# Kernel tuning notes

Measured on AMD Instinct MI355X. Metric: run time of the kernel, lower is better.

## Reference

```python
import jax, jax.numpy as jnp
import numpy as np

B, N, F_IN, H, FO = 4, 2048, 256, 4, 64


def setup_inputs() -> dict:
    key = jax.random.key(0)
    k1, k2, k3, k4, k5 = jax.random.split(key, 5)
    x = jax.random.normal(k1, (B, N, F_IN), dtype=jnp.float32)
    # random 0/1 adjacency with self-loops so every row of softmax is finite
    adj = jax.random.randint(k2, (N, N), 0, 2).astype(jnp.float32)
    adj = jnp.maximum(adj, jnp.eye(N, dtype=jnp.float32))
    # parameters (xavier-uniform style)
    lim_w = float(np.sqrt(6.0 / (F_IN + H * FO)))
    W = jax.random.uniform(k3, (F_IN, H * FO), minval=-lim_w, maxval=lim_w, dtype=jnp.float32)
    lim_a = float(np.sqrt(6.0 / (H + FO)))
    a_src = jax.random.uniform(k4, (H, FO), minval=-lim_a, maxval=lim_a, dtype=jnp.float32)
    a_dst = jax.random.uniform(k5, (H, FO), minval=-lim_a, maxval=lim_a, dtype=jnp.float32)
    return {"x": x, "adj": adj, "W": W, "a_src": a_src, "a_dst": a_dst}


def reference(x, adj, W, a_src, a_dst):
    # h: (B, N, H, FO)
    h = (x @ W).reshape(B, N, H, FO)
    attn_src = jnp.einsum("bnhf,hf->bnh", h, a_src)  # (B,N,H)
    attn_dst = jnp.einsum("bnhf,hf->bnh", h, a_dst)  # (B,N,H)
    # scores[b,i,j,h] = src[b,i,h] + dst[b,j,h]
    scores = attn_src[:, :, None, :] + attn_dst[:, None, :, :]
    scores = jax.nn.leaky_relu(scores, negative_slope=0.2)
    mask = (adj == 0)[None, :, :, None]  # (1,N,N,1)
    scores = jnp.where(mask, -jnp.inf, scores)
    attn = jax.nn.softmax(scores, axis=2)  # softmax over neighbors j
    # dropout is identity in eval mode / p=0
    out = jnp.einsum("bijh,bjhf->bihf", attn, h)  # (B,N,H,FO)
    return out.reshape(B, N, H * FO)  # concat=True
```

## Files before the change

### kernel.cpp

```cpp
#include <hip/hip_runtime.h>
#include <hip/hip_bf16.h>
#include <math.h>

#define B 4
#define N 2048
#define FIN 256
#define H 4
#define FO 64
#define M (B*N)
#define HF (H*FO)

typedef __attribute__((ext_vector_type(8))) short short8;
typedef __attribute__((ext_vector_type(4))) float float4v;
typedef __attribute__((ext_vector_type(4))) int int4v;

#if __has_builtin(__builtin_amdgcn_exp2f)
#define EXP2(x) __builtin_amdgcn_exp2f(x)
#else
#define EXP2(x) exp2f(x)
#endif

static __device__ __forceinline__ unsigned int pk_rne(float a, float b) {
  unsigned int ua = __builtin_bit_cast(unsigned int, a);
  unsigned int ub = __builtin_bit_cast(unsigned int, b);
  ua += 0x7fffu + ((ua >> 16) & 1u);
  ub += 0x7fffu + ((ub >> 16) & 1u);
  return (ua >> 16) | (ub & 0xffff0000u);
}

static __device__ __forceinline__ unsigned int pk_trunc(float a, float b) {
#if __has_builtin(__builtin_amdgcn_perm)
  return __builtin_amdgcn_perm(__builtin_bit_cast(unsigned int, b),
                               __builtin_bit_cast(unsigned int, a), 0x07060302u);
#else
  return (__builtin_bit_cast(unsigned int, a) >> 16) |
         (__builtin_bit_cast(unsigned int, b) & 0xffff0000u);
#endif
}

static __device__ __forceinline__ void split_pair(float x0, float x1,
                                                  unsigned int& hi, unsigned int& lo) {
  unsigned int u0 = __builtin_bit_cast(unsigned int, x0);
  unsigned int u1 = __builtin_bit_cast(unsigned int, x1);
  hi = (u0 >> 16) | (u1 & 0xffff0000u);
  float h0 = __builtin_bit_cast(float, u0 & 0xffff0000u);
  float h1 = __builtin_bit_cast(float, u1 & 0xffff0000u);
  unsigned int l0 = __builtin_bit_cast(unsigned int, x0 - h0);
  unsigned int l1 = __builtin_bit_cast(unsigned int, x1 - h1);
  lo = (l0 >> 16) | (l1 & 0xffff0000u);
}

static __device__ __forceinline__ unsigned int fenc(float f) {
  unsigned int b = __builtin_bit_cast(unsigned int, f);
  return (b & 0x80000000u) ? ~b : (b | 0x80000000u);
}
static __device__ __forceinline__ float fdec(unsigned int e) {
  unsigned int b = (e & 0x80000000u) ? (e & 0x7fffffffu) : ~e;
  return __builtin_bit_cast(float, b);
}

__global__ __launch_bounds__(256) void prep_pack(const float* __restrict__ Wsrc,
                                                 const float* __restrict__ X,
                                                 const float* __restrict__ adj,
                                                 unsigned short* __restrict__ Wf_hi,
                                                 unsigned short* __restrict__ Wf_lo,
                                                 unsigned short* __restrict__ Xf_hi,
                                                 unsigned short* __restrict__ Xf_lo,
                                                 unsigned long long* __restrict__ packed,
                                                 unsigned int* __restrict__ DmaxEnc) {
  const int blk = blockIdx.x;
  const int t = threadIdx.x;
  if (blk >= 144) {
    const int row = blk - 144;
    const int w = t >> 6, l = t & 63;
    const float* ar = adj + (size_t)row * N;
    for (int c = w; c < N / 64; c += 4) {
      unsigned long long m = __ballot(ar[c * 64 + l] != 0.f);
      if (l == 0) packed[(size_t)row * (N / 64) + c] = m;
    }
    return;
  }
  __shared__ float lds[64][65];
  if (blk < 16) {
    if (blk == 0 && t < 16) DmaxEnc[t] = 0u;
    const int k0 = (blk >> 2) * 64;
    const int h  = blk & 3;
    const int n0 = h * 64;
    const int c4 = (t & 15) * 4;
    #pragma unroll
    for (int rep = 0; rep < 4; ++rep) {
      const int kl = (t >> 4) + 16 * rep;
      const float4 v = *(const float4*)(Wsrc + (size_t)(k0 + kl) * HF + n0 + c4);
      lds[kl][c4 + 0] = v.x; lds[kl][c4 + 1] = v.y;
      lds[kl][c4 + 2] = v.z; lds[kl][c4 + 3] = v.w;
    }
    __syncthreads();
    #pragma unroll
    for (int rep = 0; rep < 2; ++rep) {
      const int s   = t + rep * 256;
      const int kcl = s >> 8;
      const int tt  = (s >> 6) & 3;
      const int ln  = s & 63;
      const int fL  = tt * 16 + (ln & 15);
      const int kb  = kcl * 32 + (ln >> 4) * 8;
      unsigned int hv[4], lv[4];
      #pragma unroll
      for (int p = 0; p < 4; ++p)
        split_pair(lds[kb + 2 * p][fL], lds[kb + 2 * p + 1][fL], hv[p], lv[p]);
      const size_t off = ((((size_t)h * 8 + (k0 >> 5) + kcl) * 4 + tt) << 9) + ln * 8;
      *(uint4*)(Wf_hi + off) = make_uint4(hv[0], hv[1], hv[2], hv[3]);
      *(uint4*)(Wf_lo + off) = make_uint4(lv[0], lv[1], lv[2], lv[3]);
    }
    return;
  }
  const int xblk  = blk - 16;
  const int mrow0 = xblk * 64;
  for (int ktile = 0; ktile < 4; ++ktile) {
    if (ktile) __syncthreads();
    const int k0 = ktile * 64;
    const int c4 = (t & 15) * 4;
    #pragma unroll
    for (int rep = 0; rep < 4; ++rep) {
      const int rl = (t >> 4) + 16 * rep;
      const float4 v = *(const float4*)(X + (size_t)(mrow0 + rl) * FIN + k0 + c4);
      lds[rl][c4 + 0] = v.x; lds[rl][c4 + 1] = v.y;
      lds[rl][c4 + 2] = v.z; lds[rl][c4 + 3] = v.w;
    }
    __syncthreads();
    #pragma unroll
    for (int rep = 0; rep < 2; ++rep) {
      const int s   = t + rep * 256;
      const int mt  = s >> 7;
      const int kcl = (s >> 6) & 1;
      const int ln  = s & 63;
      const int mrl = mt * 16 + (ln & 15);
      const int kb  = kcl * 32 + (ln >> 4) * 8;
      unsigned int hv[4], lv[4];
      #pragma unroll
      for (int p = 0; p < 4; ++p)
        split_pair(lds[mrl][kb + 2 * p], lds[mrl][kb + 2 * p + 1], hv[p], lv[p]);
      const size_t off = (((size_t)(xblk * 4 + mt) * 8 + (ktile * 2 + kcl)) << 9) + ln * 8;
      *(uint4*)(Xf_hi + off) = make_uint4(hv[0], hv[1], hv[2], hv[3]);
      *(uint4*)(Xf_lo + off) = make_uint4(lv[0], lv[1], lv[2], lv[3]);
    }
  }
}

__global__ __launch_bounds__(256) void gemm_fused(const unsigned short* __restrict__ Xf_hi,
                                                  const unsigned short* __restrict__ Xf_lo,
                                                  const unsigned short* __restrict__ Wf_hi,
                                                  const unsigned short* __restrict__ Wf_lo,
                                                  const float* __restrict__ a_src,
                                                  const float* __restrict__ a_dst,
                                                  float* __restrict__ Srcv,
                                                  float2* __restrict__ Epair,
                                                  unsigned int* __restrict__ DmaxEnc,
                                                  unsigned short* __restrict__ Hf) {
  __shared__ unsigned short sh[64][72];
  __shared__ float smax[4];
  const int xcd  = blockIdx.x & 7;
  const int slot = blockIdx.x >> 3;
  const int mb = xcd * 16 + (slot >> 2);
  const int h  = slot & 3;
  const int w = threadIdx.x >> 6, lane = threadIdx.x & 63;
  const int fl = lane & 15, quad = lane >> 4;
  const float L2E = 1.4426950408889634f;

  const float4v zero = {0.f, 0.f, 0.f, 0.f};
  float4v acc[4] = {zero, zero, zero, zero};

  const size_t abase = (((size_t)(mb * 4 + w) * 8) << 9) + lane * 8;
  #pragma unroll
  for (int kc = 0; kc < 8; ++kc) {
    const short8 Ahi = *(const short8*)(Xf_hi + abase + ((size_t)kc << 9));
    const short8 Alo = *(const short8*)(Xf_lo + abase + ((size_t)kc << 9));
    #pragma unroll
    for (int t = 0; t < 4; ++t) {
      const size_t woff = ((((size_t)h * 8 + kc) * 4 + t) << 9) + lane * 8;
      const short8 Bhi = *(const short8*)(Wf_hi + woff);
      const short8 Blo = *(const short8*)(Wf_lo + woff);
      acc[t] = __builtin_amdgcn_mfma_f32_16x16x32_bf16(Ahi, Bhi, acc[t], 0, 0, 0);
      acc[t] = __builtin_amdgcn_mfma_f32_16x16x32_bf16(Alo, Bhi, acc[t], 0, 0, 0);
      acc[t] = __builtin_amdgcn_mfma_f32_16x16x32_bf16(Ahi, Blo, acc[t], 0, 0, 0);
    }
  }

  const int bb  = (mb * 64) >> 11;
  const int n0w = (mb * 64) & (N - 1);
  const int bh  = bb * H + h;
  float as[4], ad[4];
  #pragma unroll
  for (int t = 0; t < 4; ++t) {
    as[t] = a_src[h * FO + t * 16 + fl];
    ad[t] = a_dst[h * FO + t * 16 + fl];
  }
  float wmax = -INFINITY;
  #pragma unroll
  for (int reg = 0; reg < 4; ++reg) {
    float sv = 0.f, dv = 0.f;
    #pragma unroll
    for (int t = 0; t < 4; ++t) {
      sv = fmaf(acc[t][reg], as[t], sv);
      dv = fmaf(acc[t][reg], ad[t], dv);
    }
    #pragma unroll
    for (int off = 1; off <= 8; off <<= 1) {
      sv += __shfl_xor(sv, off, 64);
      dv += __shfl_xor(dv, off, 64);
    }
    wmax = fmaxf(wmax, dv);
    if (fl == 0) {
      const int node = n0w + w * 16 + quad * 4 + reg;
      Srcv[(bh << 11) + node] = sv;
      float2 e;
      e.x = EXP2(dv * L2E);
      e.y = EXP2(dv * (0.2f * L2E));
      Epair[(bh << 11) + node] = e;
    }
  }
  wmax = fmaxf(wmax, __shfl_xor(wmax, 16, 64));
  wmax = fmaxf(wmax, __shfl_xor(wmax, 32, 64));
  if (lane == 0) smax[w] = wmax;

  #pragma unroll
  for (int t = 0; t < 4; ++t) {
    const int nl = w * 16 + quad * 4;
    *(unsigned int*)&sh[t * 16 + fl][nl]     = pk_rne(acc[t][0], acc[t][1]);
    *(unsigned int*)&sh[t * 16 + fl][nl + 2] = pk_rne(acc[t][2], acc[t][3]);
  }
  __syncthreads();
  if (threadIdx.x == 0) {
    const float bmax = fmaxf(fmaxf(smax[0], smax[1]), fmaxf(smax[2], smax[3]));
    atomicMax(DmaxEnc + bh, fenc(bmax));
  }
  const int jc0 = n0w >> 5;
  #pragma unroll
  for (int rep = 0; rep < 2; ++rep) {
    const int s = (int)threadIdx.x + rep * 256;
    const int jcl = s >> 8;
    const int tt  = (s >> 6) & 3;
    const int ln  = s & 63;
    const int f    = tt * 16 + (ln & 15);
    const int node = jcl * 32 + (ln >> 4) * 8;
    unsigned short* dsth = Hf + (((size_t)bh * 64 + jc0 + jcl) * 4 + tt) * 512 + ln * 8;
    *(uint4*)dsth = *(const uint4*)&sh[f][node];
  }
}

__global__ __launch_bounds__(512) void gat_mfma(const unsigned char* __restrict__ pb,
                                                const float* __restrict__ Src,
                                                const float2* __restrict__ Epair,
                                                const unsigned int* __restrict__ DmaxEnc,
                                                const unsigned short* __restrict__ Hf,
                                                float* __restrict__ out) {
  const int xcd  = blockIdx.x & 7;
  const int slot = blockIdx.x >> 3;
  const int b    = xcd >> 1;
  const int i0   = ((xcd & 1) * 32 + slot) * 32;
  const int w    = threadIdx.x >> 6;
  const int lane = threadIdx.x & 63;
  const int h    = w & 3;
  const int jh   = w >> 2;
  const int bh   = b * H + h;
  const int fl   = lane & 15;
  const int kk   = (lane >> 4) * 8;
  const float L2E = 1.4426950408889634f;

  const int row0 = i0 + fl;
  const int row1 = i0 + 16 + fl;
  const float dmx = fdec(DmaxEnc[bh]);
  const float s0 = Src[(bh << 11) + row0];
  const float s1 = Src[(bh << 11) + row1];
  const float u0 = s0 + dmx, m0 = fmaxf(u0, 0.2f * u0);
  const float u1 = s1 + dmx, m1 = fmaxf(u1, 0.2f * u1);
  const float c1a = EXP2((s0 - m0) * L2E), c2a = EXP2((0.2f * s0 - m0) * L2E);
  const float c1b = EXP2((s1 - m1) * L2E), c2b = EXP2((0.2f * s1 - m1) * L2E);
  const float ta = EXP2(-s0 * L2E), tb = EXP2(-s1 * L2E);
  const float* ep = (const float*)(Epair + (bh << 11));
  const unsigned char* pb0 = pb + (size_t)row0 * (N / 8);
  const unsigned char* pb1 = pb + (size_t)row1 * (N / 8);
  const unsigned short* hfb = Hf + (size_t)bh * 64 * 2048 + lane * 8;

  const short onebf = 0x3F80;
  short8 ones;
  #pragma unroll
  for (int jj = 0; jj < 8; ++jj) ones[jj] = onebf;

  const float4v zero = {0.f, 0.f, 0.f, 0.f};
  float4v acc[2][4];
  float4v accL[2];
  #pragma unroll
  for (int rt = 0; rt < 2; ++rt) {
    accL[rt] = zero;
    #pragma unroll
    for (int t = 0; t < 4; ++t) acc[rt][t] = zero;
  }

  const int jbeg = jh * (N / 2);
  short8 nb0, nb1, nb2, nb3;
  float4 nq0, nq1, nq2, nq3;
  unsigned int nm0, nm1;
  {
    const unsigned short* hc = hfb + (size_t)(jbeg >> 5) * 2048;
    nb0 = *(const short8*)(hc + 0 * 512);
    nb1 = *(const short8*)(hc + 1 * 512);
    nb2 = *(const short8*)(hc + 2 * 512);
    nb3 = *(const short8*)(hc + 3 * 512);
    nq0 = *(const float4*)(ep + 2 * (jbeg + kk) + 0);
    nq1 = *(const float4*)(ep + 2 * (jbeg + kk) + 4);
    nq2 = *(const float4*)(ep + 2 * (jbeg + kk) + 8);
    nq3 = *(const float4*)(ep + 2 * (jbeg + kk) + 12);
    nm0 = pb0[(jbeg + kk) >> 3];
    nm1 = pb1[(jbeg + kk) >> 3];
  }

  for (int it = 0; it < 32; ++it) {
    const short8 b0 = nb0, b1 = nb1, b2 = nb2, b3 = nb3;
    const float4 q0 = nq0, q1 = nq1, q2 = nq2, q3 = nq3;
    const unsigned int mk0 = nm0, mk1 = nm1;
    if (it < 31) {
      const int jn = jbeg + (it + 1) * 32;
      const unsigned short* hc = hfb + (size_t)(jn >> 5) * 2048;
      nb0 = *(const short8*)(hc + 0 * 512);
      nb1 = *(const short8*)(hc + 1 * 512);
      nb2 = *(const short8*)(hc + 2 * 512);
      nb3 = *(const short8*)(hc + 3 * 512);
      nq0 = *(const float4*)(ep + 2 * (jn + kk) + 0);
      nq1 = *(const float4*)(ep + 2 * (jn + kk) + 4);
      nq2 = *(const float4*)(ep + 2 * (jn + kk) + 8);
      nq3 = *(const float4*)(ep + 2 * (jn + kk) + 12);
      nm0 = pb0[(jn + kk) >> 3];
      nm1 = pb1[(jn + kk) >> 3];
    }
    const float E1v[8] = {q0.x, q0.z, q1.x, q1.z, q2.x, q2.z, q3.x, q3.z};
    const float E2v[8] = {q0.y, q0.w, q1.y, q1.w, q2.y, q2.w, q3.y, q3.w};
    int p0i[4], p1i[4];
    #pragma unroll
    for (int p = 0; p < 4; ++p) {
      const int e0 = 2 * p, e1 = 2 * p + 1;
      const bool sa0 = E1v[e0] > ta;
      float va0 = (sa0 ? c1a : c2a) * (sa0 ? E1v[e0] : E2v[e0]);
      va0 = ((mk0 >> e0) & 1u) ? va0 : 0.f;
      const bool sa1 = E1v[e1] > ta;
      float va1 = (sa1 ? c1a : c2a) * (sa1 ? E1v[e1] : E2v[e1]);
      va1 = ((mk0 >> e1) & 1u) ? va1 : 0.f;
      p0i[p] = (int)pk_trunc(va0, va1);
      const bool sb0 = E1v[e0] > tb;
      float vb0 = (sb0 ? c1b : c2b) * (sb0 ? E1v[e0] : E2v[e0]);
      vb0 = ((mk1 >> e0) & 1u) ? vb0 : 0.f;
      const bool sb1 = E1v[e1] > tb;
      float vb1 = (sb1 ? c1b : c2b) * (sb1 ? E1v[e1] : E2v[e1]);
      vb1 = ((mk1 >> e1) & 1u) ? vb1 : 0.f;
      p1i[p] = (int)pk_trunc(vb0, vb1);
    }
    const short8 p0 = __builtin_bit_cast(short8, (int4v){p0i[0], p0i[1], p0i[2], p0i[3]});
    const short8 p1 = __builtin_bit_cast(short8, (int4v){p1i[0], p1i[1], p1i[2], p1i[3]});
    acc[0][0] = __builtin_amdgcn_mfma_f32_16x16x32_bf16(p0, b0, acc[0][0], 0, 0, 0);
    acc[0][1] = __builtin_amdgcn_mfma_f32_16x16x32_bf16(p0, b1, acc[0][1], 0, 0, 0);
    acc[0][2] = __builtin_amdgcn_mfma_f32_16x16x32_bf16(p0, b2, acc[0][2], 0, 0, 0);
    acc[0][3] = __builtin_amdgcn_mfma_f32_16x16x32_bf16(p0, b3, acc[0][3], 0, 0, 0);
    accL[0]   = __builtin_amdgcn_mfma_f32_16x16x32_bf16(p0, ones, accL[0], 0, 0, 0);
    acc[1][0] = __builtin_amdgcn_mfma_f32_16x16x32_bf16(p1, b0, acc[1][0], 0, 0, 0);
    acc[1][1] = __builtin_amdgcn_mfma_f32_16x16x32_bf16(p1, b1, acc[1][1], 0, 0, 0);
    acc[1][2] = __builtin_amdgcn_mfma_f32_16x16x32_bf16(p1, b2, acc[1][2], 0, 0, 0);
    acc[1][3] = __builtin_amdgcn_mfma_f32_16x16x32_bf16(p1, b3, acc[1][3], 0, 0, 0);
    accL[1]   = __builtin_amdgcn_mfma_f32_16x16x32_bf16(p1, ones, accL[1], 0, 0, 0);
  }

  __shared__ float4v parts[4][64][11];
  if (jh == 1) {
    #pragma unroll
    for (int rt = 0; rt < 2; ++rt) {
      #pragma unroll
      for (int t = 0; t < 4; ++t) parts[h][lane][rt * 5 + t] = acc[rt][t];
      parts[h][lane][rt * 5 + 4] = accL[rt];
    }
  }
  __syncthreads();
  if (jh == 0) {
    #pragma unroll
    for (int rt = 0; rt < 2; ++rt) {
      #pragma unroll
      for (int t = 0; t < 4; ++t) acc[rt][t] += parts[h][lane][rt * 5 + t];
      accL[rt] += parts[h][lane][rt * 5 + 4];
    }
    const int quad = lane >> 4;
    #pragma unroll
    for (int rt = 0; rt < 2; ++rt) {
      #pragma unroll
      for (int reg = 0; reg < 4; ++reg) {
        const int r = i0 + rt * 16 + quad * 4 + reg;
        const float invl = 1.f / accL[rt][reg];
        float* op = out + ((size_t)(b * N) + r) * HF + h * FO + fl;
        #pragma unroll
        for (int t = 0; t < 4; ++t) op[t * 16] = acc[rt][t][reg] * invl;
      }
    }
  }
}

extern "C" void kernel_launch(void* const* d_in, const int* in_sizes, int n_in,
                              void* d_out, int out_size, void* d_ws, size_t ws_size,
                              hipStream_t stream) {
  const float* x     = (const float*)d_in[0];
  const float* adj   = (const float*)d_in[1];
  const float* W     = (const float*)d_in[2];
  const float* a_src = (const float*)d_in[3];
  const float* a_dst = (const float*)d_in[4];
  float* out = (float*)d_out;

  char* p = (char*)d_ws;
  float* Srcv = (float*)p;                 p += (size_t)B * H * N * 4;
  float2* Epair = (float2*)p;              p += (size_t)B * H * N * 8;
  unsigned int* DmaxEnc = (unsigned int*)p; p += 256;
  unsigned short* Wfh = (unsigned short*)p; p += (size_t)HF * FIN * 2;
  unsigned short* Wfl = (unsigned short*)p; p += (size_t)HF * FIN * 2;
  unsigned short* Xfh = (unsigned short*)p; p += (size_t)M * FIN * 2;
  unsigned short* Xfl = (unsigned short*)p; p += (size_t)M * FIN * 2;
  unsigned short* Hf  = (unsigned short*)p; p += (size_t)M * HF * 2;
  unsigned long long* packed = (unsigned long long*)p;

  prep_pack<<<dim3(144 + N), dim3(256), 0, stream>>>(W, x, adj, Wfh, Wfl, Xfh, Xfl,
                                                     packed, DmaxEnc);
  gemm_fused<<<dim3((M / 64) * H), dim3(256), 0, stream>>>(Xfh, Xfl, Wfh, Wfl,
                                                           a_src, a_dst,
                                                           Srcv, Epair, DmaxEnc, Hf);
  gat_mfma<<<dim3(B * (N / 32)), dim3(512), 0, stream>>>((const unsigned char*)packed,
                                                         Srcv, Epair, DmaxEnc, Hf, out);
}
```

Before: 131.0 us.

## Split GAT neighbor loop four ways, prefetch GEMM operands, branchless leaky-relu weights

The attention kernel now runs 1024 threads per block, and each head's neighbor range is split into four quarters instead of two. Partial accumulators are combined through a serial shared-memory reduction that needs several barriers. The goal is more waves per CU to hide load latency in a grid of only 256 blocks. The GEMM kernel double-buffers its A and W fragment loads one k-chunk ahead, and the per-edge weight uses fmax of two products in place of a compare and select, which is valid because exp is monotonic. The costs are higher register pressure under the 1024-thread launch bound and the extra reduction barriers.

```diff
diff --git a/kernel.cpp b/kernel.cpp
--- a/kernel.cpp
+++ b/kernel.cpp
@@ -170,18 +170,37 @@
   float4v acc[4] = {zero, zero, zero, zero};
 
   const size_t abase = (((size_t)(mb * 4 + w) * 8) << 9) + lane * 8;
+  const size_t wbase = (((size_t)h * 8) * 4 << 9) + lane * 8;
+
+  short8 nAhi = *(const short8*)(Xf_hi + abase);
+  short8 nAlo = *(const short8*)(Xf_lo + abase);
+  short8 nBhi[4], nBlo[4];
+  #pragma unroll
+  for (int t = 0; t < 4; ++t) {
+    nBhi[t] = *(const short8*)(Wf_hi + wbase + ((size_t)t << 9));
+    nBlo[t] = *(const short8*)(Wf_lo + wbase + ((size_t)t << 9));
+  }
   #pragma unroll
   for (int kc = 0; kc < 8; ++kc) {
-    const short8 Ahi = *(const short8*)(Xf_hi + abase + ((size_t)kc << 9));
-    const short8 Alo = *(const short8*)(Xf_lo + abase + ((size_t)kc << 9));
+    const short8 Ahi = nAhi, Alo = nAlo;
+    short8 Bhi[4], Blo[4];
+    #pragma unroll
+    for (int t = 0; t < 4; ++t) { Bhi[t] = nBhi[t]; Blo[t] = nBlo[t]; }
+    if (kc < 7) {
+      nAhi = *(const short8*)(Xf_hi + abase + ((size_t)(kc + 1) << 9));
+      nAlo = *(const short8*)(Xf_lo + abase + ((size_t)(kc + 1) << 9));
+      #pragma unroll
+      for (int t = 0; t < 4; ++t) {
+        const size_t woff = wbase + ((size_t)((kc + 1) * 4 + t) << 9);
+        nBhi[t] = *(const short8*)(Wf_hi + woff);
+        nBlo[t] = *(const short8*)(Wf_lo + woff);
+      }
+    }
     #pragma unroll
     for (int t = 0; t < 4; ++t) {
-      const size_t woff = ((((size_t)h * 8 + kc) * 4 + t) << 9) + lane * 8;
-      const short8 Bhi = *(const short8*)(Wf_hi + woff);
-      const short8 Blo = *(const short8*)(Wf_lo + woff);
-      acc[t] = __builtin_amdgcn_mfma_f32_16x16x32_bf16(Ahi, Bhi, acc[t], 0, 0, 0);
-      acc[t] = __builtin_amdgcn_mfma_f32_16x16x32_bf16(Alo, Bhi, acc[t], 0, 0, 0);
-      acc[t] = __builtin_amdgcn_mfma_f32_16x16x32_bf16(Ahi, Blo, acc[t], 0, 0, 0);
+      acc[t] = __builtin_amdgcn_mfma_f32_16x16x32_bf16(Ahi, Bhi[t], acc[t], 0, 0, 0);
+      acc[t] = __builtin_amdgcn_mfma_f32_16x16x32_bf16(Alo, Bhi[t], acc[t], 0, 0, 0);
+      acc[t] = __builtin_amdgcn_mfma_f32_16x16x32_bf16(Ahi, Blo[t], acc[t], 0, 0, 0);
     }
   }
 
@@ -247,12 +266,12 @@
   }
 }
 
-__global__ __launch_bounds__(512) void gat_mfma(const unsigned char* __restrict__ pb,
-                                                const float* __restrict__ Src,
-                                                const float2* __restrict__ Epair,
-                                                const unsigned int* __restrict__ DmaxEnc,
-                                                const unsigned short* __restrict__ Hf,
-                                                float* __restrict__ out) {
+__global__ __launch_bounds__(1024) void gat_mfma(const unsigned char* __restrict__ pb,
+                                                 const float* __restrict__ Src,
+                                                 const float2* __restrict__ Epair,
+                                                 const unsigned int* __restrict__ DmaxEnc,
+                                                 const unsigned short* __restrict__ Hf,
+                                                 float* __restrict__ out) {
   const int xcd  = blockIdx.x & 7;
   const int slot = blockIdx.x >> 3;
   const int b    = xcd >> 1;
@@ -260,7 +279,7 @@
   const int w    = threadIdx.x >> 6;
   const int lane = threadIdx.x & 63;
   const int h    = w & 3;
-  const int jh   = w >> 2;
+  const int q    = w >> 2;
   const int bh   = b * H + h;
   const int fl   = lane & 15;
   const int kk   = (lane >> 4) * 8;
@@ -275,7 +294,6 @@
   const float u1 = s1 + dmx, m1 = fmaxf(u1, 0.2f * u1);
   const float c1a = EXP2((s0 - m0) * L2E), c2a = EXP2((0.2f * s0 - m0) * L2E);
   const float c1b = EXP2((s1 - m1) * L2E), c2b = EXP2((0.2f * s1 - m1) * L2E);
-  const float ta = EXP2(-s0 * L2E), tb = EXP2(-s1 * L2E);
   const float* ep = (const float*)(Epair + (bh << 11));
   const unsigned char* pb0 = pb + (size_t)row0 * (N / 8);
   const unsigned char* pb1 = pb + (size_t)row1 * (N / 8);
@@ -296,7 +314,7 @@
     for (int t = 0; t < 4; ++t) acc[rt][t] = zero;
   }
 
-  const int jbeg = jh * (N / 2);
+  const int jbeg = q * (N / 4);
   short8 nb0, nb1, nb2, nb3;
   float4 nq0, nq1, nq2, nq3;
   unsigned int nm0, nm1;
@@ -314,11 +332,11 @@
     nm1 = pb1[(jbeg + kk) >> 3];
   }
 
-  for (int it = 0; it < 32; ++it) {
+  for (int it = 0; it < 16; ++it) {
     const short8 b0 = nb0, b1 = nb1, b2 = nb2, b3 = nb3;
     const float4 q0 = nq0, q1 = nq1, q2 = nq2, q3 = nq3;
     const unsigned int mk0 = nm0, mk1 = nm1;
-    if (it < 31) {
+    if (it < 15) {
       const int jn = jbeg + (it + 1) * 32;
       const unsigned short* hc = hfb + (size_t)(jn >> 5) * 2048;
       nb0 = *(const short8*)(hc + 0 * 512);
@@ -338,18 +356,14 @@
     #pragma unroll
     for (int p = 0; p < 4; ++p) {
       const int e0 = 2 * p, e1 = 2 * p + 1;
-      const bool sa0 = E1v[e0] > ta;
-      float va0 = (sa0 ? c1a : c2a) * (sa0 ? E1v[e0] : E2v[e0]);
+      float va0 = fmaxf(c1a * E1v[e0], c2a * E2v[e0]);
       va0 = ((mk0 >> e0) & 1u) ? va0 : 0.f;
-      const bool sa1 = E1v[e1] > ta;
-      float va1 = (sa1 ? c1a : c2a) * (sa1 ? E1v[e1] : E2v[e1]);
+      float va1 = fmaxf(c1a * E1v[e1], c2a * E2v[e1]);
       va1 = ((mk0 >> e1) & 1u) ? va1 : 0.f;
       p0i[p] = (int)pk_trunc(va0, va1);
-      const bool sb0 = E1v[e0] > tb;
-      float vb0 = (sb0 ? c1b : c2b) * (sb0 ? E1v[e0] : E2v[e0]);
+      float vb0 = fmaxf(c1b * E1v[e0], c2b * E2v[e0]);
       vb0 = ((mk1 >> e0) & 1u) ? vb0 : 0.f;
-      const bool sb1 = E1v[e1] > tb;
-      float vb1 = (sb1 ? c1b : c2b) * (sb1 ? E1v[e1] : E2v[e1]);
+      float vb1 = fmaxf(c1b * E1v[e1], c2b * E2v[e1]);
       vb1 = ((mk1 >> e1) & 1u) ? vb1 : 0.f;
       p1i[p] = (int)pk_trunc(vb0, vb1);
     }
@@ -368,22 +382,28 @@
   }
 
   __shared__ float4v parts[4][64][11];
-  if (jh == 1) {
-    #pragma unroll
-    for (int rt = 0; rt < 2; ++rt) {
-      #pragma unroll
-      for (int t = 0; t < 4; ++t) parts[h][lane][rt * 5 + t] = acc[rt][t];
-      parts[h][lane][rt * 5 + 4] = accL[rt];
-    }
-  }
-  __syncthreads();
-  if (jh == 0) {
-    #pragma unroll
-    for (int rt = 0; rt < 2; ++rt) {
-      #pragma unroll
-      for (int t = 0; t < 4; ++t) acc[rt][t] += parts[h][lane][rt * 5 + t];
-      accL[rt] += parts[h][lane][rt * 5 + 4];
-    }
+  for (int r = 3; r >= 1; --r) {
+    if (q == r) {
+      #pragma unroll
+      for (int rt = 0; rt < 2; ++rt) {
+        #pragma unroll
+        for (int t = 0; t < 4; ++t) parts[h][lane][rt * 5 + t] = acc[rt][t];
+        parts[h][lane][rt * 5 + 4] = accL[rt];
+      }
+    }
+    __syncthreads();
+    if (q == r - 1) {
+      #pragma unroll
+      for (int rt = 0; rt < 2; ++rt) {
+        #pragma unroll
+        for (int t = 0; t < 4; ++t) acc[rt][t] += parts[h][lane][rt * 5 + t];
+        accL[rt] += parts[h][lane][rt * 5 + 4];
+      }
+    }
+    __syncthreads();
+  }
+
+  if (q == 0) {
     const int quad = lane >> 4;
     #pragma unroll
     for (int rt = 0; rt < 2; ++rt) {
@@ -425,6 +445,6 @@
   gemm_fused<<<dim3((M / 64) * H), dim3(256), 0, stream>>>(Xfh, Xfl, Wfh, Wfl,
                                                            a_src, a_dst,
                                                            Srcv, Epair, DmaxEnc, Hf);
-  gat_mfma<<<dim3(B * (N / 32)), dim3(512), 0, stream>>>((const unsigned char*)packed,
-                                                         Srcv, Epair, DmaxEnc, Hf, out);
-}
+  gat_mfma<<<dim3(B * (N / 32)), dim3(1024), 0, stream>>>((const unsigned char*)packed,
+                                                          Srcv, Epair, DmaxEnc, Hf, out);
+}
```

Result: no change. 133.4 us (+1.9%).
